# Kernel tuning notes

Measured on AMD Instinct MI355X. Metric: run time of the kernel, lower is better.

## Reference

```python
import jax, jax.numpy as jnp
import numpy as np
from jax import lax

N, IN_CH, OUT_CH, KERNEL, D = 16, 256, 256, 3, 4096
FACTOR = 2  # upsampling factor
RESAMPLE_K = (1.0, 3.0, 3.0, 1.0)


def _fir_kernel():
    # _setup_kernel: normalize to sum 1; upsample path scales by gain * factor
    k = np.asarray(RESAMPLE_K, dtype=np.float32)
    k = k / k.sum()
    return k * FACTOR  # gain = 1


def setup_inputs() -> dict:
    key = jax.random.key(0)
    k1, k2, k3 = jax.random.split(key, 3)
    x = jax.random.normal(k1, (N, IN_CH, D), dtype=jnp.float32)
    weight = jax.random.normal(k2, (OUT_CH, IN_CH, KERNEL), dtype=jnp.float32) * 0.05
    bias = jax.random.normal(k3, (OUT_CH,), dtype=jnp.float32) * 0.05
    return {"x": x, "weight": weight, "bias": bias}


def _upfirdn1d(x, k, pad0, pad1):
    # up=down=1 path of StyleGAN2 upfirdn1d: pad, then TRUE convolution with FIR k
    # (torch native impl flips k before F.conv1d). Depthwise via [N*C,1,L] reshape.
    n, c, _ = x.shape
    xp = jnp.pad(x, ((0, 0), (0, 0), (pad0, pad1)))
    kr = k[::-1][None, None, :]  # flip -> correlation == convolution
    y = lax.conv_general_dilated(
        xp.reshape(n * c, 1, -1), kr, window_strides=(1,), padding=[(0, 0)],
        dimension_numbers=("NCH", "OIH", "NCH"))
    return y.reshape(n, c, -1)


def _upsample_conv_1d(x, w):
    # torch: w reshaped/flipped/permuted then conv_transpose1d(stride=factor).
    # conv_transpose with that transformed weight == correlation with the ORIGINAL
    # w on an input dilated by `factor` with (convH-1) padding on both sides
    # (output_padding = 0 for these shapes).
    convH = w.shape[2]
    y = lax.conv_general_dilated(
        x, w, window_strides=(1,), padding=[(convH - 1, convH - 1)],
        lhs_dilation=(FACTOR,), dimension_numbers=("NCH", "OIH", "NCH"))
    k = jnp.asarray(_fir_kernel())
    p = k.shape[0] - FACTOR - (convH - 1)  # = 0 here
    pad0 = (p + 1) // 2 + FACTOR - 1
    pad1 = p // 2 + 1
    return _upfirdn1d(y, k, pad0, pad1)  # -> [N, C_out, D * FACTOR]


def reference(x, weight, bias):
    y = _upsample_conv_1d(x, weight)
    return y + bias[None, :, None]
```

## Files before the change

kernel.cpp:

```cpp
#include <hip/hip_runtime.h>
#include <hip/hip_bf16.h>

#define N_   16
#define CI_  256
#define CO_  256
#define D_   4096
#define DO_  8192
#define KTOT 768
#define XTROWS 4098
#define WT_ELEMS (512 * KTOT)
#define XT_ELEMS ((size_t)N_ * XTROWS * 256)

typedef short frag8 __attribute__((ext_vector_type(8)));
typedef float facc4 __attribute__((ext_vector_type(4)));

static __device__ __forceinline__ unsigned short f2bf(float f) {
    union { __hip_bfloat16 h; unsigned short u; } cv;
    cv.h = __float2bfloat16(f);
    return cv.u;
}

static __device__ __forceinline__ unsigned int pack2(float lo, float hi) {
    return (unsigned int)f2bf(lo) | ((unsigned int)f2bf(hi) << 16);
}

static __device__ __forceinline__ void async16(unsigned short* lds, const unsigned short* g) {
    __builtin_amdgcn_global_load_lds(
        (const __attribute__((address_space(1))) unsigned int*)g,
        (__attribute__((address_space(3))) unsigned int*)lds, 16, 0, 0);
}

#define DSR_(dst, addr, litstr) \
    asm volatile("ds_read_b128 %0, %1 offset:" litstr : "=&v"(dst) : "v"(addr))

__global__ __launch_bounds__(256) void prep_all(const float* __restrict__ x,
                                                const float* __restrict__ w,
                                                unsigned short* __restrict__ Wt,
                                                unsigned short* __restrict__ xt) {
    const int tid = threadIdx.x;

    if (blockIdx.x == 128) {
        const int ci = tid;
        #pragma unroll 2
        for (int i = 0; i < 16; ++i) {
            const int co = blockIdx.y * 16 + i;
            const float* wp = w + ((size_t)co * CI_ + ci) * 3;
            const float w0 = wp[0], w1 = wp[1], w2 = wp[2];
            const float e0 = 0.25f * w1 + 0.75f * w0;
            const float e1 = 0.75f * w2 + 0.75f * w1 + 0.25f * w0;
            const float e2 = 0.25f * w2;
            const float o0 = 0.25f * w0;
            const float o1 = 0.25f * w2 + 0.75f * w1 + 0.75f * w0;
            const float o2 = 0.75f * w2 + 0.25f * w1;
            unsigned short* pe = Wt + (size_t)(co * 2 + 0) * KTOT;
            unsigned short* po = Wt + (size_t)(co * 2 + 1) * KTOT;
            pe[0 * 256 + ci] = f2bf(e0); pe[1 * 256 + ci] = f2bf(e1); pe[2 * 256 + ci] = f2bf(e2);
            po[0 * 256 + ci] = f2bf(o0); po[1 * 256 + ci] = f2bf(o1); po[2 * 256 + ci] = f2bf(o2);
        }
        return;
    }

    __shared__ unsigned int Lp[32][133];
    const int t0  = blockIdx.x * 32;
    const int n   = blockIdx.y;
    const float* xn = x + (size_t)n * CI_ * D_;
    unsigned short* slab = xt + (size_t)n * XTROWS * 256;

    if (t0 == 0 && tid < 128)       ((unsigned int*)slab)[tid] = 0u;
    if (t0 == D_ - 32 && tid < 128) ((unsigned int*)(slab + (size_t)(XTROWS - 1) * 256))[tid] = 0u;

    const int cp_l  = tid >> 3;
    const int t_off = (tid & 7) * 4;

    #pragma unroll
    for (int p = 0; p < 4; ++p) {
        const int ci0 = p * 64 + cp_l * 2;
        float4 a = *(const float4*)(xn + (size_t)ci0 * D_ + t0 + t_off);
        float4 b = *(const float4*)(xn + (size_t)(ci0 + 1) * D_ + t0 + t_off);
        const int cp = p * 32 + cp_l;
        Lp[t_off + 0][cp] = pack2(a.x, b.x);
        Lp[t_off + 1][cp] = pack2(a.y, b.y);
        Lp[t_off + 2][cp] = pack2(a.z, b.z);
        Lp[t_off + 3][cp] = pack2(a.w, b.w);
    }
    __syncthreads();

    #pragma unroll
    for (int it = 0; it < 4; ++it) {
        const int row = it * 8 + (tid >> 5);
        const int c4  = (tid & 31) * 4;
        uint4 v;
        v.x = Lp[row][c4 + 0];
        v.y = Lp[row][c4 + 1];
        v.z = Lp[row][c4 + 2];
        v.w = Lp[row][c4 + 3];
        *(uint4*)(slab + (size_t)(1 + t0 + row) * 256 + c4 * 2) = v;
    }
}

__global__ __launch_bounds__(512, 2) void gemm_upfir8(
    const unsigned short* __restrict__ Wt, const unsigned short* __restrict__ xt,
    const float* __restrict__ bias, float* __restrict__ out)
{
    __shared__ __align__(16) unsigned short SL[65536];

    const int tid  = threadIdx.x;
    const int lane = tid & 63;
    const int wid  = tid >> 6;
    const int quad = lane >> 4;
    const int l16  = lane & 15;

    const int bt0 = blockIdx.x * 256;
    const int bm0 = blockIdx.y * 256;
    const int n   = blockIdx.z;

    const int srow = wid * 16 + (lane >> 2);
    const int cg   = (lane & 3) ^ ((lane >> 3) & 3);
    const unsigned short* sA = Wt + (size_t)(bm0 + srow) * KTOT + cg * 8;
    const unsigned short* sB = xt + (size_t)n * XTROWS * 256
                                  + (size_t)(bt0 + srow) * 256 + cg * 8;

    #define STAGE_A(u, mh) do {                                                     \
        async16(SL + (((u)&1)*16384 + (mh)*8192 + 0*4096 + wid*512),                \
                sA + (size_t)(mh)*128*KTOT + (u)*64 + 0);                           \
        async16(SL + (((u)&1)*16384 + (mh)*8192 + 1*4096 + wid*512),                \
                sA + (size_t)(mh)*128*KTOT + (u)*64 + 32); } while (0)
    #define STAGE_B(u, th) do {                                                     \
        async16(SL + (32768 + ((u)&1)*16384 + (th)*8192 + 0*4096 + wid*512),        \
                sB + (size_t)(th)*128*256 + (u)*64 + 0);                            \
        async16(SL + (32768 + ((u)&1)*16384 + (th)*8192 + 1*4096 + wid*512),        \
                sB + (size_t)(th)*128*256 + (u)*64 + 32); } while (0)

    const int swz = quad ^ ((l16 >> 1) & 3);
    const int mh  = wid & 1;
    const int wm  = mh * 128;
    const int wt  = ((wid >> 1) & 3) * 64;
    const unsigned base = (unsigned)(size_t)&SL[0];
    const unsigned aB = base + (unsigned)(mh * 16384 + l16 * 64 + swz * 16);
    const unsigned bB = base + 65536u
                      + (unsigned)(((wid >> 2) & 1) * 16384
                                   + (((wid >> 1) & 1) * 64 + l16) * 64 + swz * 16);

    facc4 acc[8][4] = {};

    STAGE_A(0, 0); STAGE_A(0, 1); STAGE_B(0, 0); STAGE_B(0, 1);
    STAGE_A(1, 0); STAGE_A(1, 1);
    asm volatile("s_waitcnt vmcnt(4)" ::: "memory");
    __builtin_amdgcn_s_barrier();

    #define MM(m, t)                                                                 \
        acc[m][t] = __builtin_amdgcn_mfma_f32_16x16x32_bf16(a[m][0], b[t][0], acc[m][t], 0, 0, 0); \
        acc[m][t] = __builtin_amdgcn_mfma_f32_16x16x32_bf16(a[m][1], b[t][1], acc[m][t], 0, 0, 0);
    #define MMROW(m) MM(m,0) MM(m,1) MM(m,2) MM(m,3)

    #define LGKM(lit) \
        asm volatile("s_waitcnt lgkmcnt(" lit ")" ::: "memory"); \
        __builtin_amdgcn_sched_barrier(0);

    #pragma unroll 2
    for (int u = 0; u < 12; ++u) {
        const unsigned au = aB + (unsigned)((u & 1) << 15);
        const unsigned bu = bB + (unsigned)((u & 1) << 15);
        frag8 a[8][2], b[4][2];

        DSR_(b[0][0], bu, "0");    DSR_(b[0][1], bu, "8192");
        DSR_(b[1][0], bu, "1024"); DSR_(b[1][1], bu, "9216");
        DSR_(b[2][0], bu, "2048"); DSR_(b[2][1], bu, "10240");
        DSR_(b[3][0], bu, "3072"); DSR_(b[3][1], bu, "11264");
        DSR_(a[0][0], au, "0");    DSR_(a[0][1], au, "8192");
        DSR_(a[1][0], au, "1024"); DSR_(a[1][1], au, "9216");
        DSR_(a[2][0], au, "2048"); DSR_(a[2][1], au, "10240");
        DSR_(a[3][0], au, "3072"); DSR_(a[3][1], au, "11264");

        LGKM("6")
        __builtin_amdgcn_s_setprio(1);
        MMROW(0)
        __builtin_amdgcn_s_setprio(0);
        LGKM("4")
        __builtin_amdgcn_s_setprio(1);
        MMROW(1)
        __builtin_amdgcn_s_setprio(0);

        DSR_(a[4][0], au, "4096"); DSR_(a[4][1], au, "12288");
        DSR_(a[5][0], au, "5120"); DSR_(a[5][1], au, "13312");
        DSR_(a[6][0], au, "6144"); DSR_(a[6][1], au, "14336");
        DSR_(a[7][0], au, "7168"); DSR_(a[7][1], au, "15360");

        LGKM("10")
        __builtin_amdgcn_s_setprio(1);
        MMROW(2)
        __builtin_amdgcn_s_setprio(0);
        LGKM("8")
        __builtin_amdgcn_s_setprio(1);
        MMROW(3)
        __builtin_amdgcn_s_setprio(0);

        LGKM("0")
        __builtin_amdgcn_s_barrier();

        if (u < 11) { STAGE_B(u + 1, 0); STAGE_B(u + 1, 1); }
        if (u < 10) { STAGE_A(u + 2, 0); STAGE_A(u + 2, 1); }

        __builtin_amdgcn_s_setprio(1);
        MMROW(4) MMROW(5) MMROW(6) MMROW(7)
        __builtin_amdgcn_s_setprio(0);

        if (u < 10) { asm volatile("s_waitcnt vmcnt(4)" ::: "memory"); }
        else        { asm volatile("s_waitcnt vmcnt(0)" ::: "memory"); }
        __builtin_amdgcn_s_barrier();
    }
    #undef MM
    #undef MMROW
    #undef LGKM
    #undef STAGE_A
    #undef STAGE_B

    #pragma unroll
    for (int m8 = 0; m8 < 8; ++m8) {
        int m0  = bm0 + wm + m8 * 16 + quad * 4;
        int co0 = m0 >> 1;
        float b0 = bias[co0];
        float b1 = bias[co0 + 1];
        #pragma unroll
        for (int t4 = 0; t4 < 4; ++t4) {
            int t = bt0 + wt + t4 * 16 + l16;
            facc4 v = acc[m8][t4];
            float* p0 = out + ((size_t)(n * CO_ + co0)) * DO_ + 2 * t;
            float* p1 = p0 + DO_;
            *(float2*)p0 = make_float2(v.x + b0, v.y + b0);
            *(float2*)p1 = make_float2(v.z + b1, v.w + b1);
        }
    }
}

__global__ __launch_bounds__(256) void upconv_fir_f32(
    const float* __restrict__ x, const float* __restrict__ w,
    const float* __restrict__ bias, float* __restrict__ out)
{
    __shared__ float ws[CI_][4];
    const int tid = threadIdx.x;
    const int co  = blockIdx.y;
    const int n   = blockIdx.z;
    {
        const float* wc = w + (size_t)co * CI_ * 3;
        ws[tid][0] = wc[tid * 3 + 0];
        ws[tid][1] = wc[tid * 3 + 1];
        ws[tid][2] = wc[tid * 3 + 2];
        ws[tid][3] = 0.f;
    }
    __syncthreads();
    const int t0 = (blockIdx.x * 256 + tid) * 8;
    const float* xn = x + (size_t)n * CI_ * D_;
    float s[10], g[9];
    #pragma unroll
    for (int k = 0; k < 10; ++k) s[k] = 0.f;
    #pragma unroll
    for (int k = 0; k < 9; ++k) g[k] = 0.f;
    #pragma unroll 2
    for (int ci = 0; ci < CI_; ++ci) {
        const float* xr = xn + ci * D_;
        float4 va = *(const float4*)(xr + t0);
        float4 vb = *(const float4*)(xr + t0 + 4);
        float  xm = (t0 > 0)      ? xr[t0 - 1] : 0.f;
        float  xp = (t0 + 8 < D_) ? xr[t0 + 8] : 0.f;
        float4 wv = *(const float4*)(&ws[ci][0]);
        const float w0 = wv.x, w1 = wv.y, w2 = wv.z;
        float xa[10];
        xa[0] = xm; xa[1] = va.x; xa[2] = va.y; xa[3] = va.z; xa[4] = va.w;
        xa[5] = vb.x; xa[6] = vb.y; xa[7] = vb.z; xa[8] = vb.w; xa[9] = xp;
        #pragma unroll
        for (int k = 0; k < 10; ++k) s[k] += w1 * xa[k];
        #pragma unroll
        for (int k = 0; k < 9; ++k)  g[k] += w0 * xa[k] + w2 * xa[k + 1];
    }
    const float b = bias[co];
    float o16[16];
    #pragma unroll
    for (int tt = 0; tt < 8; ++tt) {
        o16[2 * tt]     = 0.25f * (s[tt] + g[tt + 1]) + 0.75f * (g[tt] + s[tt + 1]) + b;
        o16[2 * tt + 1] = 0.25f * (g[tt] + s[tt + 2]) + 0.75f * (s[tt + 1] + g[tt + 1]) + b;
    }
    float* ob = out + ((size_t)n * CO_ + co) * DO_ + 2 * t0;
    *(float4*)(ob + 0)  = make_float4(o16[0],  o16[1],  o16[2],  o16[3]);
    *(float4*)(ob + 4)  = make_float4(o16[4],  o16[5],  o16[6],  o16[7]);
    *(float4*)(ob + 8)  = make_float4(o16[8],  o16[9],  o16[10], o16[11]);
    *(float4*)(ob + 12) = make_float4(o16[12], o16[13], o16[14], o16[15]);
}

extern "C" void kernel_launch(void* const* d_in, const int* in_sizes, int n_in,
                              void* d_out, int out_size, void* d_ws, size_t ws_size,
                              hipStream_t stream) {
    const float* x  = (const float*)d_in[0];
    const float* w  = (const float*)d_in[1];
    const float* b  = (const float*)d_in[2];
    float* out      = (float*)d_out;

    const size_t need = (size_t)WT_ELEMS * 2 + XT_ELEMS * 2;
    if (ws_size >= need) {
        unsigned short* Wt = (unsigned short*)d_ws;
        unsigned short* xt = Wt + WT_ELEMS;
        prep_all<<<dim3(D_ / 32 + 1, N_), 256, 0, stream>>>(x, w, Wt, xt);
        gemm_upfir8<<<dim3(D_ / 256, 2, N_), 512, 0, stream>>>(Wt, xt, b, out);
    } else {
        upconv_fir_f32<<<dim3(2, CO_, N_), 256, 0, stream>>>(x, w, b, out);
    }
}
```

Measured before the change: 234.7 us.

## Load B operand fragments directly from global into registers, halving LDS

The GEMM kernel stops staging the activation (B) tiles through shared memory. Each wave now loads its own B fragments from global memory straight into a double-buffered register array, prefetching one k-step ahead, and the LDS footprint drops to half. The MFMA schedule is reorganised into three LDS-wait groups plus a post-barrier group, with adjusted vmcnt thresholds and a fully unrolled k loop. This removes LDS writes and reads and the bank traffic for B. In exchange it adds redundant global loads, since waves sharing the same time columns each fetch them, along with more register pressure and exposed global latency.

Result: slower. 257.4 us (+9.7%).

```diff
diff --git a/kernel.cpp b/kernel.cpp
--- a/kernel.cpp
+++ b/kernel.cpp
@@ -98,11 +98,11 @@
     }
 }
 
-__global__ __launch_bounds__(512, 2) void gemm_upfir8(
+__global__ __launch_bounds__(512, 2) void gemm_bdir(
     const unsigned short* __restrict__ Wt, const unsigned short* __restrict__ xt,
     const float* __restrict__ bias, float* __restrict__ out)
 {
-    __shared__ __align__(16) unsigned short SL[65536];
+    __shared__ __align__(16) unsigned short SL[32768];
 
     const int tid  = threadIdx.x;
     const int lane = tid & 63;
@@ -117,19 +117,12 @@
     const int srow = wid * 16 + (lane >> 2);
     const int cg   = (lane & 3) ^ ((lane >> 3) & 3);
     const unsigned short* sA = Wt + (size_t)(bm0 + srow) * KTOT + cg * 8;
-    const unsigned short* sB = xt + (size_t)n * XTROWS * 256
-                                  + (size_t)(bt0 + srow) * 256 + cg * 8;
 
     #define STAGE_A(u, mh) do {                                                     \
         async16(SL + (((u)&1)*16384 + (mh)*8192 + 0*4096 + wid*512),                \
                 sA + (size_t)(mh)*128*KTOT + (u)*64 + 0);                           \
         async16(SL + (((u)&1)*16384 + (mh)*8192 + 1*4096 + wid*512),                \
                 sA + (size_t)(mh)*128*KTOT + (u)*64 + 32); } while (0)
-    #define STAGE_B(u, th) do {                                                     \
-        async16(SL + (32768 + ((u)&1)*16384 + (th)*8192 + 0*4096 + wid*512),        \
-                sB + (size_t)(th)*128*256 + (u)*64 + 0);                            \
-        async16(SL + (32768 + ((u)&1)*16384 + (th)*8192 + 1*4096 + wid*512),        \
-                sB + (size_t)(th)*128*256 + (u)*64 + 32); } while (0)
 
     const int swz = quad ^ ((l16 >> 1) & 3);
     const int mh  = wid & 1;
@@ -137,83 +130,89 @@
     const int wt  = ((wid >> 1) & 3) * 64;
     const unsigned base = (unsigned)(size_t)&SL[0];
     const unsigned aB = base + (unsigned)(mh * 16384 + l16 * 64 + swz * 16);
-    const unsigned bB = base + 65536u
-                      + (unsigned)(((wid >> 2) & 1) * 16384
-                                   + (((wid >> 1) & 1) * 64 + l16) * 64 + swz * 16);
+
+    const unsigned short* xtn = xt + (size_t)n * XTROWS * 256;
+    const unsigned short* bp[4];
+    #pragma unroll
+    for (int ti = 0; ti < 4; ++ti)
+        bp[ti] = xtn + (size_t)(bt0 + wt + ti * 16 + l16) * 256 + quad * 8;
 
     facc4 acc[8][4] = {};
-
-    STAGE_A(0, 0); STAGE_A(0, 1); STAGE_B(0, 0); STAGE_B(0, 1);
+    frag8 bbuf[2][4][2];
+
+    STAGE_A(0, 0); STAGE_A(0, 1);
     STAGE_A(1, 0); STAGE_A(1, 1);
-    asm volatile("s_waitcnt vmcnt(4)" ::: "memory");
+    #pragma unroll
+    for (int ti = 0; ti < 4; ++ti) {
+        bbuf[0][ti][0] = *(const frag8*)(bp[ti] + 0);
+        bbuf[0][ti][1] = *(const frag8*)(bp[ti] + 32);
+    }
+    asm volatile("s_waitcnt vmcnt(12)" ::: "memory");
     __builtin_amdgcn_s_barrier();
 
     #define MM(m, t)                                                                 \
-        acc[m][t] = __builtin_amdgcn_mfma_f32_16x16x32_bf16(a[m][0], b[t][0], acc[m][t], 0, 0, 0); \
-        acc[m][t] = __builtin_amdgcn_mfma_f32_16x16x32_bf16(a[m][1], b[t][1], acc[m][t], 0, 0, 0);
+        acc[m][t] = __builtin_amdgcn_mfma_f32_16x16x32_bf16(a[m][0], bbuf[u & 1][t][0], acc[m][t], 0, 0, 0); \
+        acc[m][t] = __builtin_amdgcn_mfma_f32_16x16x32_bf16(a[m][1], bbuf[u & 1][t][1], acc[m][t], 0, 0, 0);
     #define MMROW(m) MM(m,0) MM(m,1) MM(m,2) MM(m,3)
 
     #define LGKM(lit) \
         asm volatile("s_waitcnt lgkmcnt(" lit ")" ::: "memory"); \
         __builtin_amdgcn_sched_barrier(0);
 
-    #pragma unroll 2
+    #pragma unroll
     for (int u = 0; u < 12; ++u) {
         const unsigned au = aB + (unsigned)((u & 1) << 15);
-        const unsigned bu = bB + (unsigned)((u & 1) << 15);
-        frag8 a[8][2], b[4][2];
-
-        DSR_(b[0][0], bu, "0");    DSR_(b[0][1], bu, "8192");
-        DSR_(b[1][0], bu, "1024"); DSR_(b[1][1], bu, "9216");
-        DSR_(b[2][0], bu, "2048"); DSR_(b[2][1], bu, "10240");
-        DSR_(b[3][0], bu, "3072"); DSR_(b[3][1], bu, "11264");
+        frag8 a[8][2];
+
+        if (u < 11) {
+            #pragma unroll
+            for (int ti = 0; ti < 4; ++ti) {
+                bbuf[(u + 1) & 1][ti][0] = *(const frag8*)(bp[ti] + (u + 1) * 64);
+                bbuf[(u + 1) & 1][ti][1] = *(const frag8*)(bp[ti] + (u + 1) * 64 + 32);
+            }
+        }
+
         DSR_(a[0][0], au, "0");    DSR_(a[0][1], au, "8192");
         DSR_(a[1][0], au, "1024"); DSR_(a[1][1], au, "9216");
         DSR_(a[2][0], au, "2048"); DSR_(a[2][1], au, "10240");
         DSR_(a[3][0], au, "3072"); DSR_(a[3][1], au, "11264");
-
-        LGKM("6")
-        __builtin_amdgcn_s_setprio(1);
-        MMROW(0)
-        __builtin_amdgcn_s_setprio(0);
         LGKM("4")
         __builtin_amdgcn_s_setprio(1);
-        MMROW(1)
+        MMROW(0) MMROW(1)
         __builtin_amdgcn_s_setprio(0);
 
         DSR_(a[4][0], au, "4096"); DSR_(a[4][1], au, "12288");
         DSR_(a[5][0], au, "5120"); DSR_(a[5][1], au, "13312");
+        LGKM("4")
+        __builtin_amdgcn_s_setprio(1);
+        MMROW(2) MMROW(3)
+        __builtin_amdgcn_s_setprio(0);
+
         DSR_(a[6][0], au, "6144"); DSR_(a[6][1], au, "14336");
         DSR_(a[7][0], au, "7168"); DSR_(a[7][1], au, "15360");
-
-        LGKM("10")
+        LGKM("4")
         __builtin_amdgcn_s_setprio(1);
-        MMROW(2)
-        __builtin_amdgcn_s_setprio(0);
-        LGKM("8")
-        __builtin_amdgcn_s_setprio(1);
-        MMROW(3)
+        MMROW(4) MMROW(5)
         __builtin_amdgcn_s_setprio(0);
 
         LGKM("0")
         __builtin_amdgcn_s_barrier();
 
-        if (u < 11) { STAGE_B(u + 1, 0); STAGE_B(u + 1, 1); }
         if (u < 10) { STAGE_A(u + 2, 0); STAGE_A(u + 2, 1); }
 
         __builtin_amdgcn_s_setprio(1);
-        MMROW(4) MMROW(5) MMROW(6) MMROW(7)
+        MMROW(6) MMROW(7)
         __builtin_amdgcn_s_setprio(0);
 
-        if (u < 10) { asm volatile("s_waitcnt vmcnt(4)" ::: "memory"); }
-        else        { asm volatile("s_waitcnt vmcnt(0)" ::: "memory"); }
+        if (u < 10)       { asm volatile("s_waitcnt vmcnt(12)" ::: "memory"); }
+        else if (u == 10) { asm volatile("s_waitcnt vmcnt(8)"  ::: "memory"); }
+        else              { asm volatile("s_waitcnt vmcnt(0)"  ::: "memory"); }
         __builtin_amdgcn_s_barrier();
     }
     #undef MM
     #undef MMROW
     #undef LGKM
     #undef STAGE_A
-    #undef STAGE_B
 
     #pragma unroll
     for (int m8 = 0; m8 < 8; ++m8) {
@@ -300,7 +299,7 @@
         unsigned short* Wt = (unsigned short*)d_ws;
         unsigned short* xt = Wt + WT_ELEMS;
         prep_all<<<dim3(D_ / 32 + 1, N_), 256, 0, stream>>>(x, w, Wt, xt);
-        gemm_upfir8<<<dim3(D_ / 256, 2, N_), 512, 0, stream>>>(Wt, xt, b, out);
+        gemm_bdir<<<dim3(D_ / 256, 2, N_), 512, 0, stream>>>(Wt, xt, b, out);
     } else {
         upconv_fir_f32<<<dim3(2, CO_, N_), 256, 0, stream>>>(x, w, b, out);
     }
```
